# Kernel optimization log

Measured on AMD Instinct MI355X. Metric: run time of the kernel, lower is better.

## Reference

```python
import jax, jax.numpy as jnp
import numpy as np
import math

B, S, D, H = 4, 2048, 512, 8
HD = D // H

def setup_inputs() -> dict:
    key = jax.random.key(0)
    ks = jax.random.split(key, 12)
    s_hd = 1.0 / math.sqrt(HD)
    s_d = 1.0 / math.sqrt(D)
    return {
        "q": jax.random.normal(ks[0], (B, S, D), jnp.float32),
        "k": jax.random.normal(ks[1], (B, S, D), jnp.float32),
        "v": jax.random.normal(ks[2], (B, S, D), jnp.float32),
        # torch nn.Linear(head_dim, head_dim): weight [HD, HD], bias [HD]
        "Wq": jax.random.uniform(ks[3], (HD, HD), jnp.float32, -s_hd, s_hd),
        "bq": jax.random.uniform(ks[4], (HD,), jnp.float32, -s_hd, s_hd),
        "Wk": jax.random.uniform(ks[5], (HD, HD), jnp.float32, -s_hd, s_hd),
        "bk": jax.random.uniform(ks[6], (HD,), jnp.float32, -s_hd, s_hd),
        "Wv": jax.random.uniform(ks[7], (HD, HD), jnp.float32, -s_hd, s_hd),
        "bv": jax.random.uniform(ks[8], (HD,), jnp.float32, -s_hd, s_hd),
        # output projection nn.Linear(d, d)
        "Wo": jax.random.uniform(ks[9], (D, D), jnp.float32, -s_d, s_d),
        "bo": jax.random.uniform(ks[10], (D,), jnp.float32, -s_d, s_d),
        # LayerNorm(d) affine params
        "gamma": jnp.ones((D,), jnp.float32),
        "beta": jnp.zeros((D,), jnp.float32),
    }

def _layernorm(x, gamma, beta, eps=1e-5):
    mu = jnp.mean(x, axis=-1, keepdims=True)
    var = jnp.var(x, axis=-1, keepdims=True)
    return (x - mu) * jax.lax.rsqrt(var + eps) * gamma + beta

def reference(q, k, v, Wq, bq, Wk, bk, Wv, bv, Wo, bo, gamma, beta):
    batch, q_len = q.shape[0], q.shape[1]
    # split heads: [B, L, H, HD]; per-head Linear shares one weight across heads
    Qh = q.reshape(batch, q_len, H, HD) @ Wq.T + bq
    Kh = k.reshape(batch, k.shape[1], H, HD) @ Wk.T + bk
    Vh = v.reshape(batch, v.shape[1], H, HD) @ Wv.T + bv
    # scores scaled by sqrt(d) (faithful to source, NOT sqrt(head_dim))
    scores = jnp.einsum('bqhd,bkhd->bhqk', Qh, Kh) / math.sqrt(D)
    attn = jax.nn.softmax(scores, axis=-1)
    out = jnp.einsum('bhqk,bkhd->bqhd', attn, Vh)
    concat = out.reshape(batch, q_len, D)
    lin = concat @ Wo.T + bo
    # AddNorm quirk: residual added AFTER LayerNorm (dropout = identity in eval)
    return q + _layernorm(lin, gamma, beta)
```

## Files before the change

kernel.cpp:

```cpp
#include <hip/hip_runtime.h>
#include <hip/hip_bf16.h>
#include <math.h>
#include <stdint.h>

#define B 4
#define S 2048
#define D 512
#define H 8
#define HD 64
#define R3 16

typedef __attribute__((ext_vector_type(4))) int   int4v;
typedef __attribute__((ext_vector_type(8))) short short8;
typedef __attribute__((ext_vector_type(4))) short short4v;
typedef __attribute__((ext_vector_type(4))) float f32x4;

__device__ __forceinline__ unsigned short bfr(float x) {
    __bf16 h = (__bf16)x;
    union { __bf16 b; unsigned short s; } u; u.b = h; return u.s;
}

__device__ __forceinline__ float ex2(float x) {
#if __has_builtin(__builtin_amdgcn_exp2f)
    return __builtin_amdgcn_exp2f(x);
#else
    return exp2f(x);
#endif
}

#define QSCALE 0.06377229601488305f
#define MFIX 4.0f

__global__ __launch_bounds__(256) void wcvt_kernel(
    const float* __restrict__ Wo, const float* __restrict__ Wq,
    const float* __restrict__ Wk, const float* __restrict__ Wv,
    unsigned short* __restrict__ WoB, unsigned short* __restrict__ WqB,
    unsigned short* __restrict__ WkB, unsigned short* __restrict__ WvB)
{
    int bid = blockIdx.x;
    const float* src; unsigned short* dst; int base;
    if (bid < 256)      { src = Wo; dst = WoB; base = bid * 1024; }
    else if (bid < 260) { src = Wq; dst = WqB; base = (bid - 256) * 1024; }
    else if (bid < 264) { src = Wk; dst = WkB; base = (bid - 260) * 1024; }
    else                { src = Wv; dst = WvB; base = (bid - 264) * 1024; }
    int i = base + threadIdx.x * 4;
    float4 f = *(const float4*)(src + i);
    short4v s;
    s[0] = (short)bfr(f.x); s[1] = (short)bfr(f.y);
    s[2] = (short)bfr(f.z); s[3] = (short)bfr(f.w);
    *(short4v*)(dst + i) = s;
}

__global__ __launch_bounds__(256) void qkv_mfma_kernel(
    const float* __restrict__ q, const float* __restrict__ k,
    const float* __restrict__ v,
    const unsigned short* __restrict__ WqB, const float* __restrict__ bq,
    const unsigned short* __restrict__ WkB, const float* __restrict__ bk,
    const unsigned short* __restrict__ WvB, const float* __restrict__ bv,
    unsigned short* __restrict__ Qh, unsigned short* __restrict__ Kh,
    unsigned short* __restrict__ Vh)
{
    __shared__ __align__(16) unsigned short xs[3][16 * 264];

    const int t = threadIdx.x;
    const int bid = blockIdx.x;
    const int s0 = (bid & 127) * 16;
    const int b = (bid >> 7) & 3;
    const int h0 = (bid >> 9) * 4;
    const int w = t >> 6, L = t & 63;
    const int c = L & 15, qd = L >> 4;
    const int h = h0 + w;

    const unsigned short* WB[3] = {WqB, WkB, WvB};
    const float* bs[3] = {bq, bk, bv};
    const float* Xs[3] = {q, k, v};
    unsigned short* Os[3] = {Qh, Kh, Vh};

    short8 wf[3][4][2];
    float bias[3][4];
    #pragma unroll
    for (int x = 0; x < 3; ++x)
        #pragma unroll
        for (int nt = 0; nt < 4; ++nt) {
            bias[x][nt] = bs[x][16 * nt + c];
            #pragma unroll
            for (int kc = 0; kc < 2; ++kc)
                wf[x][nt][kc] = *(const short8*)(WB[x] + (16 * nt + c) * HD + 32 * kc + 8 * qd);
        }

    #pragma unroll
    for (int x = 0; x < 3; ++x) {
        #pragma unroll
        for (int i = 0; i < 4; ++i) {
            int f = t + 256 * i;
            int row = f >> 6, col4 = f & 63;
            float4 val = *(const float4*)(Xs[x]
                + ((size_t)(b * S + s0 + row)) * D + h0 * 64 + col4 * 4);
            short4v sv;
            sv[0] = (short)bfr(val.x); sv[1] = (short)bfr(val.y);
            sv[2] = (short)bfr(val.z); sv[3] = (short)bfr(val.w);
            *(short4v*)&xs[x][row * 264 + col4 * 4] = sv;
        }
    }
    __syncthreads();

    #pragma unroll
    for (int x = 0; x < 3; ++x) {
        short8 a0 = *(const short8*)&xs[x][c * 264 + w * 64 + 8 * qd];
        short8 a1 = *(const short8*)&xs[x][c * 264 + w * 64 + 32 + 8 * qd];
        f32x4 acc[4];
        #pragma unroll
        for (int nt = 0; nt < 4; ++nt) {
            float bv_ = bias[x][nt];
            acc[nt] = (f32x4){bv_, bv_, bv_, bv_};
            acc[nt] = __builtin_amdgcn_mfma_f32_16x16x32_bf16(a0, wf[x][nt][0], acc[nt], 0, 0, 0);
            acc[nt] = __builtin_amdgcn_mfma_f32_16x16x32_bf16(a1, wf[x][nt][1], acc[nt], 0, 0, 0);
        }
        unsigned short* O = Os[x] + ((size_t)(b * H + h) * S + s0) * HD;
        #pragma unroll
        for (int nt = 0; nt < 4; ++nt)
            #pragma unroll
            for (int r = 0; r < 4; ++r) {
                float o = acc[nt][r];
                if (x == 0) o *= QSCALE;
                O[(4 * qd + r) * HD + 16 * nt + c] = bfr(o);
            }
    }
}

__global__ __launch_bounds__(512) void attn_kernel(
    const unsigned short* __restrict__ Qh, const unsigned short* __restrict__ Kh,
    const unsigned short* __restrict__ Vh, unsigned short* __restrict__ concat)
{
    __shared__ __align__(16) char Ks[8192];
    __shared__ __align__(16) char Vt[8192];

    const int idx = blockIdx.x;
    const int bh = idx >> 4;
    const int qt = idx & 15;
    const int b = bh >> 3, h = bh & 7;
    const int t = threadIdx.x;
    const int w = t >> 6;
    const int L = t & 63;
    const int c = L & 15, qd = L >> 4;

    const unsigned short* Kb = Kh + (size_t)bh * S * HD;
    const unsigned short* Vb = Vh + (size_t)bh * S * HD;

    const int qrow = qt * 128 + w * 16 + c;
    const unsigned short* Qrow = Qh + ((size_t)bh * S + qrow) * HD;
    short8 qf0 = *(const short8*)(Qrow + qd * 8);
    short8 qf1 = *(const short8*)(Qrow + 32 + qd * 8);

    f32x4 acc[4];
    #pragma unroll
    for (int i = 0; i < 4; ++i) acc[i] = (f32x4){0.f, 0.f, 0.f, 0.f};
    f32x4 accl = (f32x4){0.f, 0.f, 0.f, 0.f};

    const short4v vones = {(short)0x3F80, (short)0x3F80, (short)0x3F80, (short)0x3F80};

    const int krow = t >> 3, kcc = t & 7;
    const int nl = t & 63, d0 = 8 * (t >> 6);
    const int n3 = nl >> 3, n7b = (nl & 7) << 1;

    const int x0 = (qd ^ (c & 7)) << 4;
    const int x1 = ((4 + qd) ^ (c & 7)) << 4;

    for (int n0 = 0; n0 < S; n0 += 64) {
        __syncthreads();
        {
            int4v kv = *(const int4v*)(Kb + (size_t)(n0 + krow) * HD + kcc * 8);
            *(int4v*)(Ks + krow * 128 + ((kcc ^ (krow & 7)) << 4)) = kv;
        }
        {
            int4v vv = *(const int4v*)(Vb + (size_t)(n0 + nl) * HD + d0);
            #pragma unroll
            for (int j = 0; j < 8; ++j) {
                unsigned hv = ((unsigned)vv[j >> 1] >> (16 * (j & 1))) & 0xffffu;
                *(unsigned short*)(Vt + (d0 + j) * 128 + ((n3 ^ j) << 4) + n7b)
                    = (unsigned short)hv;
            }
        }
        __syncthreads();

        #pragma unroll
        for (int mt = 0; mt < 4; ++mt) {
            const char* rowp = Ks + (16 * mt + c) * 128;
            short8 a0 = *(const short8*)(rowp + x0);
            short8 a1 = *(const short8*)(rowp + x1);
            f32x4 st = (f32x4){-MFIX, -MFIX, -MFIX, -MFIX};
            st = __builtin_amdgcn_mfma_f32_16x16x32_bf16(a0, qf0, st, 0, 0, 0);
            st = __builtin_amdgcn_mfma_f32_16x16x32_bf16(a1, qf1, st, 0, 0, 0);

            short4v pa;
            pa[0] = (short)bfr(ex2(st[0]));
            pa[1] = (short)bfr(ex2(st[1]));
            pa[2] = (short)bfr(ex2(st[2]));
            pa[3] = (short)bfr(ex2(st[3]));

            const int vx = (((2 * mt + (qd >> 1)) ^ (c & 7)) << 4) + ((qd & 1) << 3);
#if __has_builtin(__builtin_amdgcn_mfma_f32_16x16x16bf16_1k)
            accl = __builtin_amdgcn_mfma_f32_16x16x16bf16_1k(pa, vones, accl, 0, 0, 0);
            #pragma unroll
            for (int dt = 0; dt < 4; ++dt) {
                short4v vf = *(const short4v*)(Vt + (16 * dt + c) * 128 + vx);
                acc[dt] = __builtin_amdgcn_mfma_f32_16x16x16bf16_1k(pa, vf, acc[dt], 0, 0, 0);
            }
#else
            short8 pa8 = {pa[0], pa[1], pa[2], pa[3], 0, 0, 0, 0};
            short8 on8 = {(short)0x3F80, (short)0x3F80, (short)0x3F80, (short)0x3F80, 0, 0, 0, 0};
            accl = __builtin_amdgcn_mfma_f32_16x16x32_bf16(pa8, on8, accl, 0, 0, 0);
            #pragma unroll
            for (int dt = 0; dt < 4; ++dt) {
                short4v vf = *(const short4v*)(Vt + (16 * dt + c) * 128 + vx);
                short8 vf8 = {vf[0], vf[1], vf[2], vf[3], 0, 0, 0, 0};
                acc[dt] = __builtin_amdgcn_mfma_f32_16x16x32_bf16(pa8, vf8, acc[dt], 0, 0, 0);
            }
#endif
        }
    }

    float linv[4];
    #pragma unroll
    for (int r = 0; r < 4; ++r) linv[r] = 1.f / accl[r];
    unsigned short* outb = concat
        + ((size_t)b * S + qt * 128 + w * 16 + 4 * qd) * D + h * HD + c;
    #pragma unroll
    for (int dt = 0; dt < 4; ++dt)
        #pragma unroll
        for (int r = 0; r < 4; ++r)
            outb[(size_t)r * D + 16 * dt] = bfr(acc[dt][r] * linv[r]);
}

__global__ __launch_bounds__(256) void oproj_ln_kernel(
    const unsigned short* __restrict__ concat, const unsigned short* __restrict__ WoB,
    const float* __restrict__ bo, const float* __restrict__ gamma,
    const float* __restrict__ beta, const float* __restrict__ qin,
    float* __restrict__ out)
{
    __shared__ __align__(16) unsigned short As[16 * 72];
    __shared__ float red[2][4][16];

    const int t = threadIdx.x;
    const int r0 = blockIdx.x * 16;
    const int w = t >> 6, L = t & 63;
    const int c = L & 15, qd = L >> 4;
    const int n0 = w * 128;

    f32x4 acc[8];
    #pragma unroll
    for (int nt = 0; nt < 8; ++nt) {
        float bv_ = bo[n0 + 16 * nt + c];
        acc[nt] = (f32x4){bv_, bv_, bv_, bv_};
    }

    const int srow = t >> 4, sc4 = t & 15;

    for (int kc0 = 0; kc0 < D; kc0 += 64) {
        short4v av = *(const short4v*)(concat + ((size_t)(r0 + srow)) * D + kc0 + sc4 * 4);
        *(short4v*)&As[srow * 72 + sc4 * 4] = av;
        __syncthreads();

        short8 a0 = *(const short8*)&As[c * 72 + 8 * qd];
        short8 a1 = *(const short8*)&As[c * 72 + 32 + 8 * qd];
        #pragma unroll
        for (int nt = 0; nt < 8; ++nt) {
            const unsigned short* bp = WoB + (size_t)(n0 + 16 * nt + c) * D + kc0 + 8 * qd;
            short8 b0 = *(const short8*)bp;
            short8 b1 = *(const short8*)(bp + 32);
            acc[nt] = __builtin_amdgcn_mfma_f32_16x16x32_bf16(a0, b0, acc[nt], 0, 0, 0);
            acc[nt] = __builtin_amdgcn_mfma_f32_16x16x32_bf16(a1, b1, acc[nt], 0, 0, 0);
        }
        __syncthreads();
    }

    float sm[4], sq[4];
    #pragma unroll
    for (int r = 0; r < 4; ++r) { sm[r] = 0.f; sq[r] = 0.f; }
    #pragma unroll
    for (int nt = 0; nt < 8; ++nt)
        #pragma unroll
        for (int r = 0; r < 4; ++r) {
            float x_ = acc[nt][r];
            sm[r] += x_; sq[r] += x_ * x_;
        }
    #pragma unroll
    for (int mask = 1; mask <= 8; mask <<= 1)
        #pragma unroll
        for (int r = 0; r < 4; ++r) {
            sm[r] += __shfl_xor(sm[r], mask);
            sq[r] += __shfl_xor(sq[r], mask);
        }
    if (c == 0) {
        #pragma unroll
        for (int r = 0; r < 4; ++r) {
            red[0][w][4 * qd + r] = sm[r];
            red[1][w][4 * qd + r] = sq[r];
        }
    }
    __syncthreads();

    float mu[4], rs[4];
    #pragma unroll
    for (int r = 0; r < 4; ++r) {
        int m_ = 4 * qd + r;
        float s_ = red[0][0][m_] + red[0][1][m_] + red[0][2][m_] + red[0][3][m_];
        float q_ = red[1][0][m_] + red[1][1][m_] + red[1][2][m_] + red[1][3][m_];
        float mu_ = s_ * (1.f / D);
        float var = q_ * (1.f / D) - mu_ * mu_;
        mu[r] = mu_;
        rs[r] = rsqrtf(var + 1e-5f);
    }

    #pragma unroll
    for (int nt = 0; nt < 8; ++nt) {
        int n = n0 + 16 * nt + c;
        float g = gamma[n], be = beta[n];
        #pragma unroll
        for (int r = 0; r < 4; ++r) {
            size_t gi = (size_t)(r0 + 4 * qd + r) * D + n;
            out[gi] = qin[gi] + (acc[nt][r] - mu[r]) * rs[r] * g + be;
        }
    }
}

extern "C" void kernel_launch(void* const* d_in, const int* in_sizes, int n_in,
                              void* d_out, int out_size, void* d_ws, size_t ws_size,
                              hipStream_t stream) {
    const float* q     = (const float*)d_in[0];
    const float* k     = (const float*)d_in[1];
    const float* v     = (const float*)d_in[2];
    const float* Wq    = (const float*)d_in[3];
    const float* bq    = (const float*)d_in[4];
    const float* Wk    = (const float*)d_in[5];
    const float* bk    = (const float*)d_in[6];
    const float* Wv    = (const float*)d_in[7];
    const float* bv    = (const float*)d_in[8];
    const float* Wo    = (const float*)d_in[9];
    const float* bo    = (const float*)d_in[10];
    const float* gamma = (const float*)d_in[11];
    const float* beta  = (const float*)d_in[12];
    float* out = (float*)d_out;

    const size_t NE = (size_t)B * S * D;
    unsigned short* wsu = (unsigned short*)d_ws;
    unsigned short* Qh     = wsu;
    unsigned short* Kh     = wsu + NE;
    unsigned short* Vh     = wsu + 2 * NE;
    unsigned short* concat = wsu + 3 * NE;
    unsigned short* WoB    = wsu + 4 * NE;
    unsigned short* WqB    = WoB + (size_t)D * D;
    unsigned short* WkB    = WqB + HD * HD;
    unsigned short* WvB    = WkB + HD * HD;

    hipLaunchKernelGGL(wcvt_kernel, dim3(268), dim3(256), 0, stream,
                       Wo, Wq, Wk, Wv, WoB, WqB, WkB, WvB);
    hipLaunchKernelGGL(qkv_mfma_kernel, dim3((S / 16) * B * 2), dim3(256), 0, stream,
                       q, k, v, WqB, bq, WkB, bk, WvB, bv, Qh, Kh, Vh);
    hipLaunchKernelGGL(attn_kernel, dim3(B * H * (S / 128)), dim3(512), 0, stream,
                       Qh, Kh, Vh, concat);
    hipLaunchKernelGGL(oproj_ln_kernel, dim3(B * S / 16), dim3(256), 0, stream,
                       concat, WoB, bo, gamma, beta, q, out);
}
```

Measured before the change: 218.5 us.

## Restructure QKV, attention and out-proj kernels with V-transpose and async K staging

The QKV projection now gives each wave one (x, b, h, s-tile) task, loads its A fragments straight from global memory, and writes V pre-transposed to global. Attention drops to 256 threads with each wave handling two 16-row query groups. K tiles are double-buffered into LDS through global_load_lds, and V fragments are read directly from global memory. The out-projection now processes 32 rows per block, staging the whole concat tile in LDS once and reusing each Wo fragment across two row tiles. Together these aim to cut LDS transposes, sync points and redundant weight loads, at the cost of more register pressure and uncached global V reads inside the attention loop.

```diff
diff --git a/kernel.cpp b/kernel.cpp
--- a/kernel.cpp
+++ b/kernel.cpp
@@ -8,7 +8,6 @@
 #define D 512
 #define H 8
 #define HD 64
-#define R3 16
 
 typedef __attribute__((ext_vector_type(4))) int   int4v;
 typedef __attribute__((ext_vector_type(8))) short short8;
@@ -19,7 +18,6 @@
     __bf16 h = (__bf16)x;
     union { __bf16 b; unsigned short s; } u; u.b = h; return u.s;
 }
-
 __device__ __forceinline__ float ex2(float x) {
 #if __has_builtin(__builtin_amdgcn_exp2f)
     return __builtin_amdgcn_exp2f(x);
@@ -30,6 +28,17 @@
 
 #define QSCALE 0.06377229601488305f
 #define MFIX 4.0f
+
+typedef const __attribute__((address_space(1))) unsigned char g8_t;
+typedef __attribute__((address_space(3))) unsigned char l8_t;
+__device__ __forceinline__ void gl_lds16(const unsigned short* g, unsigned short* l) {
+#if __has_builtin(__builtin_amdgcn_global_load_lds)
+    __builtin_amdgcn_global_load_lds((g8_t*)g, (l8_t*)l, 16, 0, 0);
+#else
+    int lane = threadIdx.x & 63;
+    ((int4v*)l)[lane] = *(const int4v*)g;
+#endif
+}
 
 __global__ __launch_bounds__(256) void wcvt_kernel(
     const float* __restrict__ Wo, const float* __restrict__ Wq,
@@ -58,178 +67,203 @@
     const unsigned short* __restrict__ WkB, const float* __restrict__ bk,
     const unsigned short* __restrict__ WvB, const float* __restrict__ bv,
     unsigned short* __restrict__ Qh, unsigned short* __restrict__ Kh,
-    unsigned short* __restrict__ Vh)
+    unsigned short* __restrict__ VtG)
 {
-    __shared__ __align__(16) unsigned short xs[3][16 * 264];
-
     const int t = threadIdx.x;
-    const int bid = blockIdx.x;
-    const int s0 = (bid & 127) * 16;
-    const int b = (bid >> 7) & 3;
-    const int h0 = (bid >> 9) * 4;
-    const int w = t >> 6, L = t & 63;
+    const int L = t & 63, w = t >> 6;
     const int c = L & 15, qd = L >> 4;
-    const int h = h0 + w;
-
-    const unsigned short* WB[3] = {WqB, WkB, WvB};
-    const float* bs[3] = {bq, bk, bv};
-    const float* Xs[3] = {q, k, v};
-    unsigned short* Os[3] = {Qh, Kh, Vh};
-
-    short8 wf[3][4][2];
-    float bias[3][4];
-    #pragma unroll
-    for (int x = 0; x < 3; ++x)
-        #pragma unroll
-        for (int nt = 0; nt < 4; ++nt) {
-            bias[x][nt] = bs[x][16 * nt + c];
-            #pragma unroll
-            for (int kc = 0; kc < 2; ++kc)
-                wf[x][nt][kc] = *(const short8*)(WB[x] + (16 * nt + c) * HD + 32 * kc + 8 * qd);
-        }
-
-    #pragma unroll
-    for (int x = 0; x < 3; ++x) {
-        #pragma unroll
-        for (int i = 0; i < 4; ++i) {
-            int f = t + 256 * i;
-            int row = f >> 6, col4 = f & 63;
-            float4 val = *(const float4*)(Xs[x]
-                + ((size_t)(b * S + s0 + row)) * D + h0 * 64 + col4 * 4);
-            short4v sv;
-            sv[0] = (short)bfr(val.x); sv[1] = (short)bfr(val.y);
-            sv[2] = (short)bfr(val.z); sv[3] = (short)bfr(val.w);
-            *(short4v*)&xs[x][row * 264 + col4 * 4] = sv;
-        }
-    }
-    __syncthreads();
-
-    #pragma unroll
-    for (int x = 0; x < 3; ++x) {
-        short8 a0 = *(const short8*)&xs[x][c * 264 + w * 64 + 8 * qd];
-        short8 a1 = *(const short8*)&xs[x][c * 264 + w * 64 + 32 + 8 * qd];
-        f32x4 acc[4];
-        #pragma unroll
-        for (int nt = 0; nt < 4; ++nt) {
-            float bv_ = bias[x][nt];
-            acc[nt] = (f32x4){bv_, bv_, bv_, bv_};
-            acc[nt] = __builtin_amdgcn_mfma_f32_16x16x32_bf16(a0, wf[x][nt][0], acc[nt], 0, 0, 0);
-            acc[nt] = __builtin_amdgcn_mfma_f32_16x16x32_bf16(a1, wf[x][nt][1], acc[nt], 0, 0, 0);
-        }
-        unsigned short* O = Os[x] + ((size_t)(b * H + h) * S + s0) * HD;
+    const int task = blockIdx.x * 4 + w;
+    const int st = task & 127;
+    const int h  = (task >> 7) & 7;
+    const int b  = (task >> 10) & 3;
+    const int x  = task >> 12;
+
+    const unsigned short* WB = (x == 0) ? WqB : (x == 1) ? WkB : WvB;
+    const float* bias_p      = (x == 0) ? bq  : (x == 1) ? bk  : bv;
+    const float* X           = (x == 0) ? q   : (x == 1) ? k   : v;
+
+    const float* xrow = X + ((size_t)(b * S + st * 16 + c)) * D + h * HD;
+    short8 af[2];
+    #pragma unroll
+    for (int kc = 0; kc < 2; ++kc) {
+        float4 f0 = *(const float4*)(xrow + kc * 32 + 8 * qd);
+        float4 f1 = *(const float4*)(xrow + kc * 32 + 8 * qd + 4);
+        short8 s8;
+        s8[0] = (short)bfr(f0.x); s8[1] = (short)bfr(f0.y);
+        s8[2] = (short)bfr(f0.z); s8[3] = (short)bfr(f0.w);
+        s8[4] = (short)bfr(f1.x); s8[5] = (short)bfr(f1.y);
+        s8[6] = (short)bfr(f1.z); s8[7] = (short)bfr(f1.w);
+        af[kc] = s8;
+    }
+
+    f32x4 acc[4];
+    #pragma unroll
+    for (int nt = 0; nt < 4; ++nt) {
+        float bv_ = bias_p[16 * nt + c];
+        acc[nt] = (f32x4){bv_, bv_, bv_, bv_};
+        short8 b0 = *(const short8*)(WB + (16 * nt + c) * HD + 8 * qd);
+        short8 b1 = *(const short8*)(WB + (16 * nt + c) * HD + 32 + 8 * qd);
+        acc[nt] = __builtin_amdgcn_mfma_f32_16x16x32_bf16(af[0], b0, acc[nt], 0, 0, 0);
+        acc[nt] = __builtin_amdgcn_mfma_f32_16x16x32_bf16(af[1], b1, acc[nt], 0, 0, 0);
+    }
+
+    if (x < 2) {
+        unsigned short* O = ((x == 0) ? Qh : Kh)
+                          + ((size_t)(b * H + h) * S + st * 16) * HD;
+        const float sc = (x == 0) ? QSCALE : 1.0f;
         #pragma unroll
         for (int nt = 0; nt < 4; ++nt)
             #pragma unroll
-            for (int r = 0; r < 4; ++r) {
-                float o = acc[nt][r];
-                if (x == 0) o *= QSCALE;
-                O[(4 * qd + r) * HD + 16 * nt + c] = bfr(o);
-            }
-    }
-}
-
-__global__ __launch_bounds__(512) void attn_kernel(
+            for (int r = 0; r < 4; ++r)
+                O[(4 * qd + r) * HD + 16 * nt + c] = bfr(acc[nt][r] * sc);
+    } else {
+        unsigned short* O = VtG + (size_t)(b * H + h) * HD * S;
+        #pragma unroll
+        for (int nt = 0; nt < 4; ++nt)
+            #pragma unroll
+            for (int r = 0; r < 4; ++r)
+                O[(size_t)(16 * nt + c) * S + st * 16 + 4 * qd + r] = bfr(acc[nt][r]);
+    }
+}
+
+__global__ __launch_bounds__(256) void attn_kernel(
     const unsigned short* __restrict__ Qh, const unsigned short* __restrict__ Kh,
-    const unsigned short* __restrict__ Vh, unsigned short* __restrict__ concat)
+    const unsigned short* __restrict__ VtG, unsigned short* __restrict__ concat)
 {
-    __shared__ __align__(16) char Ks[8192];
-    __shared__ __align__(16) char Vt[8192];
+    __shared__ __align__(16) unsigned short Ks[2][4096];
 
     const int idx = blockIdx.x;
     const int bh = idx >> 4;
     const int qt = idx & 15;
     const int b = bh >> 3, h = bh & 7;
     const int t = threadIdx.x;
-    const int w = t >> 6;
-    const int L = t & 63;
+    const int w = t >> 6, L = t & 63;
     const int c = L & 15, qd = L >> 4;
 
     const unsigned short* Kb = Kh + (size_t)bh * S * HD;
-    const unsigned short* Vb = Vh + (size_t)bh * S * HD;
-
-    const int qrow = qt * 128 + w * 16 + c;
-    const unsigned short* Qrow = Qh + ((size_t)bh * S + qrow) * HD;
-    short8 qf0 = *(const short8*)(Qrow + qd * 8);
-    short8 qf1 = *(const short8*)(Qrow + 32 + qd * 8);
-
-    f32x4 acc[4];
-    #pragma unroll
-    for (int i = 0; i < 4; ++i) acc[i] = (f32x4){0.f, 0.f, 0.f, 0.f};
-    f32x4 accl = (f32x4){0.f, 0.f, 0.f, 0.f};
+    const unsigned short* Vb = VtG + (size_t)bh * HD * S;
+
+    short8 qf[2][2];
+    #pragma unroll
+    for (int qg = 0; qg < 2; ++qg)
+        #pragma unroll
+        for (int kc = 0; kc < 2; ++kc)
+            qf[qg][kc] = *(const short8*)(Qh
+                + ((size_t)bh * S + qt * 128 + w * 32 + qg * 16 + c) * HD
+                + kc * 32 + 8 * qd);
+
+    f32x4 acc[2][4];
+    f32x4 accl[2];
+    #pragma unroll
+    for (int qg = 0; qg < 2; ++qg) {
+        accl[qg] = (f32x4){0.f, 0.f, 0.f, 0.f};
+        #pragma unroll
+        for (int dt = 0; dt < 4; ++dt) acc[qg][dt] = (f32x4){0.f, 0.f, 0.f, 0.f};
+    }
 
     const short4v vones = {(short)0x3F80, (short)0x3F80, (short)0x3F80, (short)0x3F80};
 
-    const int krow = t >> 3, kcc = t & 7;
-    const int nl = t & 63, d0 = 8 * (t >> 6);
-    const int n3 = nl >> 3, n7b = (nl & 7) << 1;
-
-    const int x0 = (qd ^ (c & 7)) << 4;
-    const int x1 = ((4 + qd) ^ (c & 7)) << 4;
-
-    for (int n0 = 0; n0 < S; n0 += 64) {
+    #define STAGE(n0_, buf_)                                                    \
+        {                                                                       \
+            _Pragma("unroll")                                                   \
+            for (int i_ = 0; i_ < 2; ++i_) {                                    \
+                int flat_ = t + 256 * i_;                                       \
+                int bi_ = flat_ >> 6, l_ = flat_ & 63;                          \
+                const unsigned short* src_ = Kb                                 \
+                    + (size_t)((n0_) + 16 * (bi_ >> 1) + (l_ & 15)) * HD        \
+                    + (bi_ & 1) * 32 + (l_ >> 4) * 8;                           \
+                gl_lds16(src_, &Ks[buf_][bi_ * 512]);                           \
+            }                                                                   \
+        }
+
+    STAGE(0, 0);
+
+    for (int it = 0; it < 32; ++it) {
+        const int n0 = it * 64;
         __syncthreads();
-        {
-            int4v kv = *(const int4v*)(Kb + (size_t)(n0 + krow) * HD + kcc * 8);
-            *(int4v*)(Ks + krow * 128 + ((kcc ^ (krow & 7)) << 4)) = kv;
+        if (it + 1 < 32) STAGE(n0 + 64, (it + 1) & 1);
+        const unsigned short* KsC = Ks[it & 1];
+
+        short4v vf[4][4];
+        #pragma unroll
+        for (int dt = 0; dt < 4; ++dt)
+            #pragma unroll
+            for (int mt = 0; mt < 4; ++mt)
+                vf[dt][mt] = *(const short4v*)(Vb + (size_t)(16 * dt + c) * S
+                                               + n0 + 16 * mt + 4 * qd);
+
+        f32x4 stv[2][4];
+        #pragma unroll
+        for (int mt = 0; mt < 4; ++mt) {
+            short8 a0 = *(const short8*)(KsC + (mt * 2 + 0) * 512 + L * 8);
+            short8 a1 = *(const short8*)(KsC + (mt * 2 + 1) * 512 + L * 8);
+            #pragma unroll
+            for (int qg = 0; qg < 2; ++qg) {
+                f32x4 s_ = (f32x4){-MFIX, -MFIX, -MFIX, -MFIX};
+                s_ = __builtin_amdgcn_mfma_f32_16x16x32_bf16(a0, qf[qg][0], s_, 0, 0, 0);
+                s_ = __builtin_amdgcn_mfma_f32_16x16x32_bf16(a1, qf[qg][1], s_, 0, 0, 0);
+                stv[qg][mt] = s_;
+            }
         }
-        {
-            int4v vv = *(const int4v*)(Vb + (size_t)(n0 + nl) * HD + d0);
-            #pragma unroll
-            for (int j = 0; j < 8; ++j) {
-                unsigned hv = ((unsigned)vv[j >> 1] >> (16 * (j & 1))) & 0xffffu;
-                *(unsigned short*)(Vt + (d0 + j) * 128 + ((n3 ^ j) << 4) + n7b)
-                    = (unsigned short)hv;
-            }
-        }
-        __syncthreads();
-
-        #pragma unroll
-        for (int mt = 0; mt < 4; ++mt) {
-            const char* rowp = Ks + (16 * mt + c) * 128;
-            short8 a0 = *(const short8*)(rowp + x0);
-            short8 a1 = *(const short8*)(rowp + x1);
-            f32x4 st = (f32x4){-MFIX, -MFIX, -MFIX, -MFIX};
-            st = __builtin_amdgcn_mfma_f32_16x16x32_bf16(a0, qf0, st, 0, 0, 0);
-            st = __builtin_amdgcn_mfma_f32_16x16x32_bf16(a1, qf1, st, 0, 0, 0);
-
-            short4v pa;
-            pa[0] = (short)bfr(ex2(st[0]));
-            pa[1] = (short)bfr(ex2(st[1]));
-            pa[2] = (short)bfr(ex2(st[2]));
-            pa[3] = (short)bfr(ex2(st[3]));
-
-            const int vx = (((2 * mt + (qd >> 1)) ^ (c & 7)) << 4) + ((qd & 1) << 3);
+
+        short4v pa[2][4];
+        #pragma unroll
+        for (int qg = 0; qg < 2; ++qg)
+            #pragma unroll
+            for (int mt = 0; mt < 4; ++mt) {
+                short4v p_;
+                p_[0] = (short)bfr(ex2(stv[qg][mt][0]));
+                p_[1] = (short)bfr(ex2(stv[qg][mt][1]));
+                p_[2] = (short)bfr(ex2(stv[qg][mt][2]));
+                p_[3] = (short)bfr(ex2(stv[qg][mt][3]));
+                pa[qg][mt] = p_;
+            }
+
 #if __has_builtin(__builtin_amdgcn_mfma_f32_16x16x16bf16_1k)
-            accl = __builtin_amdgcn_mfma_f32_16x16x16bf16_1k(pa, vones, accl, 0, 0, 0);
-            #pragma unroll
-            for (int dt = 0; dt < 4; ++dt) {
-                short4v vf = *(const short4v*)(Vt + (16 * dt + c) * 128 + vx);
-                acc[dt] = __builtin_amdgcn_mfma_f32_16x16x16bf16_1k(pa, vf, acc[dt], 0, 0, 0);
+        #pragma unroll
+        for (int qg = 0; qg < 2; ++qg)
+            #pragma unroll
+            for (int mt = 0; mt < 4; ++mt) {
+                accl[qg] = __builtin_amdgcn_mfma_f32_16x16x16bf16_1k(
+                    pa[qg][mt], vones, accl[qg], 0, 0, 0);
+                #pragma unroll
+                for (int dt = 0; dt < 4; ++dt)
+                    acc[qg][dt] = __builtin_amdgcn_mfma_f32_16x16x16bf16_1k(
+                        pa[qg][mt], vf[dt][mt], acc[qg][dt], 0, 0, 0);
             }
 #else
-            short8 pa8 = {pa[0], pa[1], pa[2], pa[3], 0, 0, 0, 0};
-            short8 on8 = {(short)0x3F80, (short)0x3F80, (short)0x3F80, (short)0x3F80, 0, 0, 0, 0};
-            accl = __builtin_amdgcn_mfma_f32_16x16x32_bf16(pa8, on8, accl, 0, 0, 0);
-            #pragma unroll
-            for (int dt = 0; dt < 4; ++dt) {
-                short4v vf = *(const short4v*)(Vt + (16 * dt + c) * 128 + vx);
-                short8 vf8 = {vf[0], vf[1], vf[2], vf[3], 0, 0, 0, 0};
-                acc[dt] = __builtin_amdgcn_mfma_f32_16x16x32_bf16(pa8, vf8, acc[dt], 0, 0, 0);
+        #pragma unroll
+        for (int qg = 0; qg < 2; ++qg)
+            #pragma unroll
+            for (int mt = 0; mt < 4; ++mt) {
+                short8 pa8 = {pa[qg][mt][0], pa[qg][mt][1], pa[qg][mt][2], pa[qg][mt][3],
+                              0, 0, 0, 0};
+                short8 on8 = {(short)0x3F80, (short)0x3F80, (short)0x3F80, (short)0x3F80,
+                              0, 0, 0, 0};
+                accl[qg] = __builtin_amdgcn_mfma_f32_16x16x32_bf16(pa8, on8, accl[qg], 0, 0, 0);
+                #pragma unroll
+                for (int dt = 0; dt < 4; ++dt) {
+                    short4v v_ = vf[dt][mt];
+                    short8 v8 = {v_[0], v_[1], v_[2], v_[3], 0, 0, 0, 0};
+                    acc[qg][dt] = __builtin_amdgcn_mfma_f32_16x16x32_bf16(pa8, v8, acc[qg][dt], 0, 0, 0);
+                }
             }
 #endif
-        }
-    }
-
-    float linv[4];
-    #pragma unroll
-    for (int r = 0; r < 4; ++r) linv[r] = 1.f / accl[r];
-    unsigned short* outb = concat
-        + ((size_t)b * S + qt * 128 + w * 16 + 4 * qd) * D + h * HD + c;
-    #pragma unroll
-    for (int dt = 0; dt < 4; ++dt)
-        #pragma unroll
-        for (int r = 0; r < 4; ++r)
-            outb[(size_t)r * D + 16 * dt] = bfr(acc[dt][r] * linv[r]);
+    }
+
+    unsigned short* outb = concat + ((size_t)b * S + qt * 128 + w * 32) * D + h * HD;
+    #pragma unroll
+    for (int qg = 0; qg < 2; ++qg) {
+        float linv[4];
+        #pragma unroll
+        for (int r = 0; r < 4; ++r) linv[r] = 1.f / accl[qg][r];
+        #pragma unroll
+        for (int dt = 0; dt < 4; ++dt)
+            #pragma unroll
+            for (int r = 0; r < 4; ++r)
+                outb[(size_t)(qg * 16 + 4 * qd + r) * D + 16 * dt + c]
+                    = bfr(acc[qg][dt][r] * linv[r]);
+    }
 }
 
 __global__ __launch_bounds__(256) void oproj_ln_kernel(
@@ -238,89 +272,103 @@
     const float* __restrict__ beta, const float* __restrict__ qin,
     float* __restrict__ out)
 {
-    __shared__ __align__(16) unsigned short As[16 * 72];
-    __shared__ float red[2][4][16];
+    __shared__ __align__(16) unsigned short As[32 * 520];
+    __shared__ float red[2][4][32];
 
     const int t = threadIdx.x;
-    const int r0 = blockIdx.x * 16;
+    const int r0 = blockIdx.x * 32;
     const int w = t >> 6, L = t & 63;
     const int c = L & 15, qd = L >> 4;
     const int n0 = w * 128;
 
-    f32x4 acc[8];
+    #pragma unroll
+    for (int i = 0; i < 8; ++i) {
+        int flat = t + 256 * i;
+        int row = flat >> 6, cc = flat & 63;
+        *(int4v*)&As[row * 520 + cc * 8]
+            = *(const int4v*)(concat + (size_t)(r0 + row) * D + cc * 8);
+    }
+    __syncthreads();
+
+    f32x4 acc[2][8];
     #pragma unroll
     for (int nt = 0; nt < 8; ++nt) {
         float bv_ = bo[n0 + 16 * nt + c];
-        acc[nt] = (f32x4){bv_, bv_, bv_, bv_};
-    }
-
-    const int srow = t >> 4, sc4 = t & 15;
-
-    for (int kc0 = 0; kc0 < D; kc0 += 64) {
-        short4v av = *(const short4v*)(concat + ((size_t)(r0 + srow)) * D + kc0 + sc4 * 4);
-        *(short4v*)&As[srow * 72 + sc4 * 4] = av;
-        __syncthreads();
-
-        short8 a0 = *(const short8*)&As[c * 72 + 8 * qd];
-        short8 a1 = *(const short8*)&As[c * 72 + 32 + 8 * qd];
+        acc[0][nt] = (f32x4){bv_, bv_, bv_, bv_};
+        acc[1][nt] = (f32x4){bv_, bv_, bv_, bv_};
+    }
+
+    for (int kc = 0; kc < 16; ++kc) {
+        short8 a0 = *(const short8*)&As[c * 520 + kc * 32 + 8 * qd];
+        short8 a1 = *(const short8*)&As[(16 + c) * 520 + kc * 32 + 8 * qd];
         #pragma unroll
         for (int nt = 0; nt < 8; ++nt) {
-            const unsigned short* bp = WoB + (size_t)(n0 + 16 * nt + c) * D + kc0 + 8 * qd;
-            short8 b0 = *(const short8*)bp;
-            short8 b1 = *(const short8*)(bp + 32);
-            acc[nt] = __builtin_amdgcn_mfma_f32_16x16x32_bf16(a0, b0, acc[nt], 0, 0, 0);
-            acc[nt] = __builtin_amdgcn_mfma_f32_16x16x32_bf16(a1, b1, acc[nt], 0, 0, 0);
+            short8 bf = *(const short8*)(WoB + (size_t)(n0 + 16 * nt + c) * D
+                                         + kc * 32 + 8 * qd);
+            acc[0][nt] = __builtin_amdgcn_mfma_f32_16x16x32_bf16(a0, bf, acc[0][nt], 0, 0, 0);
+            acc[1][nt] = __builtin_amdgcn_mfma_f32_16x16x32_bf16(a1, bf, acc[1][nt], 0, 0, 0);
         }
-        __syncthreads();
-    }
-
-    float sm[4], sq[4];
-    #pragma unroll
-    for (int r = 0; r < 4; ++r) { sm[r] = 0.f; sq[r] = 0.f; }
-    #pragma unroll
-    for (int nt = 0; nt < 8; ++nt)
+    }
+
+    float sm[2][4], sq[2][4];
+    #pragma unroll
+    for (int mt = 0; mt < 2; ++mt)
+        #pragma unroll
+        for (int r = 0; r < 4; ++r) { sm[mt][r] = 0.f; sq[mt][r] = 0.f; }
+    #pragma unroll
+    for (int mt = 0; mt < 2; ++mt)
+        #pragma unroll
+        for (int nt = 0; nt < 8; ++nt)
+            #pragma unroll
+            for (int r = 0; r < 4; ++r) {
+                float x_ = acc[mt][nt][r];
+                sm[mt][r] += x_; sq[mt][r] += x_ * x_;
+            }
+    #pragma unroll
+    for (int mask = 1; mask <= 8; mask <<= 1)
+        #pragma unroll
+        for (int mt = 0; mt < 2; ++mt)
+            #pragma unroll
+            for (int r = 0; r < 4; ++r) {
+                sm[mt][r] += __shfl_xor(sm[mt][r], mask);
+                sq[mt][r] += __shfl_xor(sq[mt][r], mask);
+            }
+    if (c == 0) {
+        #pragma unroll
+        for (int mt = 0; mt < 2; ++mt)
+            #pragma unroll
+            for (int r = 0; r < 4; ++r) {
+                red[0][w][16 * mt + 4 * qd + r] = sm[mt][r];
+                red[1][w][16 * mt + 4 * qd + r] = sq[mt][r];
+            }
+    }
+    __syncthreads();
+
+    float mu[2][4], rs[2][4];
+    #pragma unroll
+    for (int mt = 0; mt < 2; ++mt)
         #pragma unroll
         for (int r = 0; r < 4; ++r) {
-            float x_ = acc[nt][r];
-            sm[r] += x_; sq[r] += x_ * x_;
+            int m_ = 16 * mt + 4 * qd + r;
+            float s_ = red[0][0][m_] + red[0][1][m_] + red[0][2][m_] + red[0][3][m_];
+            float q_ = red[1][0][m_] + red[1][1][m_] + red[1][2][m_] + red[1][3][m_];
+            float mu_ = s_ * (1.f / D);
+            float var = q_ * (1.f / D) - mu_ * mu_;
+            mu[mt][r] = mu_;
+            rs[mt][r] = rsqrtf(var + 1e-5f);
         }
-    #pragma unroll
-    for (int mask = 1; mask <= 8; mask <<= 1)
-        #pragma unroll
-        for (int r = 0; r < 4; ++r) {
-            sm[r] += __shfl_xor(sm[r], mask);
-            sq[r] += __shfl_xor(sq[r], mask);
-        }
-    if (c == 0) {
-        #pragma unroll
-        for (int r = 0; r < 4; ++r) {
-            red[0][w][4 * qd + r] = sm[r];
-            red[1][w][4 * qd + r] = sq[r];
-        }
-    }
-    __syncthreads();
-
-    float mu[4], rs[4];
-    #pragma unroll
-    for (int r = 0; r < 4; ++r) {
-        int m_ = 4 * qd + r;
-        float s_ = red[0][0][m_] + red[0][1][m_] + red[0][2][m_] + red[0][3][m_];
-        float q_ = red[1][0][m_] + red[1][1][m_] + red[1][2][m_] + red[1][3][m_];
-        float mu_ = s_ * (1.f / D);
-        float var = q_ * (1.f / D) - mu_ * mu_;
-        mu[r] = mu_;
-        rs[r] = rsqrtf(var + 1e-5f);
-    }
 
     #pragma unroll
     for (int nt = 0; nt < 8; ++nt) {
         int n = n0 + 16 * nt + c;
         float g = gamma[n], be = beta[n];
         #pragma unroll
-        for (int r = 0; r < 4; ++r) {
-            size_t gi = (size_t)(r0 + 4 * qd + r) * D + n;
-            out[gi] = qin[gi] + (acc[nt][r] - mu[r]) * rs[r] * g + be;
-        }
+        for (int mt = 0; mt < 2; ++mt)
+            #pragma unroll
+            for (int r = 0; r < 4; ++r) {
+                size_t gi = (size_t)(r0 + 16 * mt + 4 * qd + r) * D + n;
+                out[gi] = qin[gi] + (acc[mt][nt][r] - mu[mt][r]) * rs[mt][r] * g + be;
+            }
     }
 }
 
@@ -346,7 +394,7 @@
     unsigned short* wsu = (unsigned short*)d_ws;
     unsigned short* Qh     = wsu;
     unsigned short* Kh     = wsu + NE;
-    unsigned short* Vh     = wsu + 2 * NE;
+    unsigned short* VtG    = wsu + 2 * NE;
     unsigned short* concat = wsu + 3 * NE;
     unsigned short* WoB    = wsu + 4 * NE;
     unsigned short* WqB    = WoB + (size_t)D * D;
@@ -355,10 +403,10 @@
 
     hipLaunchKernelGGL(wcvt_kernel, dim3(268), dim3(256), 0, stream,
                        Wo, Wq, Wk, Wv, WoB, WqB, WkB, WvB);
-    hipLaunchKernelGGL(qkv_mfma_kernel, dim3((S / 16) * B * 2), dim3(256), 0, stream,
-                       q, k, v, WqB, bq, WkB, bk, WvB, bv, Qh, Kh, Vh);
-    hipLaunchKernelGGL(attn_kernel, dim3(B * H * (S / 128)), dim3(512), 0, stream,
-                       Qh, Kh, Vh, concat);
-    hipLaunchKernelGGL(oproj_ln_kernel, dim3(B * S / 16), dim3(256), 0, stream,
+    hipLaunchKernelGGL(qkv_mfma_kernel, dim3((S / 16) * B * H * 3 / 4), dim3(256), 0, stream,
+                       q, k, v, WqB, bq, WkB, bk, WvB, bv, Qh, Kh, VtG);
+    hipLaunchKernelGGL(attn_kernel, dim3(B * H * (S / 128)), dim3(256), 0, stream,
+                       Qh, Kh, VtG, concat);
+    hipLaunchKernelGGL(oproj_ln_kernel, dim3(B * S / 32), dim3(256), 0, stream,
                        concat, WoB, bo, gamma, beta, q, out);
 }
```

Result: slower. 282.5 us (+29.3%).
